# Kernel optimization log

Measured on AMD Instinct MI355X. Metric: run time of the kernel, lower is better.

Reference implementation:

```python
import jax, jax.numpy as jnp
import numpy as np

DIM = 512
NUM_HEADS = 8


def setup_inputs() -> dict:
    key = jax.random.key(0)
    ks = jax.random.split(key, 10)
    B, N, C = 2, 4096, DIM
    s = 0.02
    return {
        "x": jax.random.normal(ks[0], (B, N, C), dtype=jnp.float32),
        "Wq": jax.random.normal(ks[1], (C, C), dtype=jnp.float32) * s,
        "Wk": jax.random.normal(ks[2], (C, C), dtype=jnp.float32) * s,
        "Wv": jax.random.normal(ks[3], (C, C), dtype=jnp.float32) * s,
        "Wattn": jax.random.normal(ks[4], (C, C), dtype=jnp.float32) * s,
        "Wconv": jax.random.normal(ks[5], (C, C), dtype=jnp.float32) * s,
        "dw_kernel": jax.random.normal(ks[6], (C, 1, 3), dtype=jnp.float32) * s,  # depthwise (O, I/groups, K)
        "dw_bias": jax.random.normal(ks[7], (C,), dtype=jnp.float32) * s,
        "Wcout": jax.random.normal(ks[8], (C, C), dtype=jnp.float32) * s,
        "H": 8,
        "W": 512,
    }


def reference(x, Wq, Wk, Wv, Wattn, Wconv, dw_kernel, dw_bias, Wcout, H, W):
    B, N, C = x.shape
    nh = NUM_HEADS
    hd = C // nh
    scale = hd ** (-0.5)

    # QKV projections (torch Linear: x @ W.T), split heads -> [B, nh, N, hd]
    q = (x @ Wq.T).reshape(B, N, nh, hd).transpose(0, 2, 1, 3)
    k = (x @ Wk.T).reshape(B, N, nh, hd).transpose(0, 2, 1, 3)
    v = (x @ Wv.T).reshape(B, N, nh, hd).transpose(0, 2, 1, 3)

    # Materialized N x N attention (faithful to source)
    scores = jnp.einsum("bhqd,bhkd->bhqk", q, k) * scale
    weights = jax.nn.softmax(scores, axis=-1)
    attn = jnp.einsum("bhqk,bhkd->bhqd", weights, v)
    attn = attn.transpose(0, 2, 1, 3).reshape(B, N, C)
    attn_out = attn @ Wattn.T

    # Parallel depthwise-conv branch
    ci = (x @ Wconv.T).transpose(0, 2, 1)  # [B, C, N]
    co = jax.lax.conv_general_dilated(
        ci, dw_kernel,
        window_strides=(1,), padding=((1, 1),),
        feature_group_count=C,
        dimension_numbers=("NCH", "OIH", "NCH"),
    ) + dw_bias[None, :, None]
    conv_out = co.transpose(0, 2, 1) @ Wcout.T  # [B, N, C]

    out = attn_out + conv_out
    # NOTE: source shadows arg H with num_heads before the view
    return out.reshape(B, nh, W, C)
```

## Files before the change

### kernel.cpp

```cpp
#include <hip/hip_runtime.h>

typedef __attribute__((ext_vector_type(8))) short bf16x8;
typedef __attribute__((ext_vector_type(4))) float f32x4;

constexpr int kB = 2, kN = 4096, kC = 512, kNH = 8, kHD = 64;
constexpr int kBN = kB * kN;
constexpr int kWElems = 262144;
constexpr int kWAll = 6 * kWElems;
constexpr int kWExtra = 3584;
constexpr float kQScale = 0.1803368801f;

__device__ __forceinline__ short f2bf(float f) {
  union { float f; unsigned u; } v; v.f = f;
  unsigned r = v.u + 0x7fffu + ((v.u >> 16) & 1u);
  return (short)(r >> 16);
}
__device__ __forceinline__ float bf2f(short s) {
  union { unsigned u; float f; } v; v.u = ((unsigned)(unsigned short)s) << 16;
  return v.f;
}
__device__ __forceinline__ float exp2_(float x) {
#if __has_builtin(__builtin_amdgcn_exp2f)
  return __builtin_amdgcn_exp2f(x);
#else
  return exp2f(x);
#endif
}
__device__ __forceinline__ unsigned pk2bf(float a, float b) {
  union { float f; unsigned u; } ua, ub; ua.f = a; ub.f = b;
#if __has_builtin(__builtin_amdgcn_perm)
  return __builtin_amdgcn_perm(ub.u + 0x8000u, ua.u + 0x8000u, 0x07060302u);
#else
  return ((ua.u + 0x8000u) >> 16) | (((ub.u + 0x8000u) >> 16) << 16);
#endif
}

__device__ __forceinline__ bf16x8 ld8(const short* p) { return *(const bf16x8*)p; }
__device__ __forceinline__ bf16x8 ld8(const float* p) {
  float4 a = *(const float4*)p;
  float4 b = *(const float4*)(p + 4);
  bf16x8 r;
  r[0] = f2bf(a.x); r[1] = f2bf(a.y); r[2] = f2bf(a.z); r[3] = f2bf(a.w);
  r[4] = f2bf(b.x); r[5] = f2bf(b.y); r[6] = f2bf(b.z); r[7] = f2bf(b.w);
  return r;
}
__device__ __forceinline__ void stf(short* p, float v) { *p = f2bf(v); }
__device__ __forceinline__ void stf(float* p, float v) { *p = v; }

__device__ __forceinline__ void gload_lds16(const void* g, void* l) {
  __builtin_amdgcn_global_load_lds(
      (const __attribute__((address_space(1))) void*)g,
      (__attribute__((address_space(3))) void*)l, 16, 0, 0);
}

__global__ void detect_dtype(const unsigned* __restrict__ x, int* __restrict__ flag) {
  const int lane = threadIdx.x & 63;
  unsigned w = x[lane];
  int e = (int)((w >> 7) & 0xffu);
  bool bf = (e >= 100 && e <= 140);
  unsigned long long m = __ballot(bf);
  if (lane == 0) *flag = (__popcll(m) >= 32) ? 1 : 0;
}

constexpr int kW8 = kWAll / 8;
constexpr int kX8 = kBN * kC / 8;
__global__ __launch_bounds__(256) void convert_all(
    const void* Wq, const void* Wk, const void* Wv, const void* Wc,
    const void* Wa, const void* Wco, const void* dwk, const void* dwb,
    const void* x, const int* __restrict__ flag, short* __restrict__ dst,
    short* __restrict__ xb) {
  const int gtid = blockIdx.x * 256 + threadIdx.x;
  const bool bf = (*flag != 0);
  if (gtid < kW8) {
    const int e = gtid * 8;
    const int t = e >> 18, off = e & (kWElems - 1);
    const void* src = (t == 0) ? Wq : (t == 1) ? Wk : (t == 2) ? Wv
                    : (t == 3) ? Wc : (t == 4) ? Wa : Wco;
    bf16x8 v = bf ? ld8((const short*)src + off) : ld8((const float*)src + off);
    *(bf16x8*)(dst + e) = v;
  } else if (gtid < kW8 + kWExtra) {
    const int eoff = gtid - kW8;
    if (eoff < 1536) {
      dst[kWAll + eoff] = bf ? ((const short*)dwk)[eoff]
                             : f2bf(((const float*)dwk)[eoff]);
    } else if (eoff < 2048) {
      const int i = eoff - 1536;
      dst[kWAll + 1536 + i] = bf ? ((const short*)dwb)[i]
                                 : f2bf(((const float*)dwb)[i]);
    } else {
      const int t2 = eoff - 2048;
      const int tap = t2 >> 9, c = t2 & 511;
      dst[kWAll + 2048 + t2] = bf ? ((const short*)dwk)[c * 3 + tap]
                                  : f2bf(((const float*)dwk)[c * 3 + tap]);
    }
  } else if (gtid < kW8 + kWExtra + kX8) {
    const int e = (gtid - kW8 - kWExtra) * 8;
    bf16x8 v = bf ? ld8((const short*)x + e) : ld8((const float*)x + e);
    *(bf16x8*)(xb + e) = v;
  }
}

__global__ __launch_bounds__(256, 3) void proj_gemm(
    const short* __restrict__ xb, const short* __restrict__ wb,
    short* __restrict__ q, short* __restrict__ k, short* __restrict__ vT,
    short* __restrict__ ci) {
  __shared__ __align__(16) short As[128 * 64];
  __shared__ __align__(16) short Bs[128 * 64];
  const int t = threadIdx.x;
  const int wave = t >> 6, lane = t & 63;
  const int row = lane & 15, quad = lane >> 4;
  const int bn = blockIdx.x & 15;
  const int bm = blockIdx.x >> 4;
  const int m0 = bm * 128, n0 = bn * 128;
  const int wm = wave & 1, wn = wave >> 1;
  const int lrow = lane >> 3, lch = lane & 7;

  f32x4 acc[4][4];
#pragma unroll
  for (int mi = 0; mi < 4; ++mi)
#pragma unroll
    for (int ni = 0; ni < 4; ++ni)
#pragma unroll
      for (int r = 0; r < 4; ++r) acc[mi][ni][r] = 0.0f;

  for (int k0 = 0; k0 < kC; k0 += 64) {
#pragma unroll
    for (int p = 0; p < 4; ++p) {
      const int m = wave * 32 + p * 8 + lrow;
      const int kch = lch ^ (m & 7);
      gload_lds16(xb + (size_t)(m0 + m) * kC + k0 + kch * 8,
                  &As[(wave * 32 + p * 8) * 64]);
      gload_lds16(wb + (size_t)(n0 + m) * kC + k0 + kch * 8,
                  &Bs[(wave * 32 + p * 8) * 64]);
    }
    __syncthreads();

#pragma unroll
    for (int kk2 = 0; kk2 < 2; ++kk2) {
      bf16x8 af[4], bfr[4];
#pragma unroll
      for (int mi = 0; mi < 4; ++mi) {
        const int m = wm * 64 + mi * 16 + row;
        const int ch = (kk2 * 4 + quad) ^ (m & 7);
        af[mi] = *(const bf16x8*)(&As[m * 64 + ch * 8]);
      }
#pragma unroll
      for (int ni = 0; ni < 4; ++ni) {
        const int n = wn * 64 + ni * 16 + row;
        const int ch = (kk2 * 4 + quad) ^ (n & 7);
        bfr[ni] = *(const bf16x8*)(&Bs[n * 64 + ch * 8]);
      }
#pragma unroll
      for (int mi = 0; mi < 4; ++mi)
#pragma unroll
        for (int ni = 0; ni < 4; ++ni)
          acc[mi][ni] = __builtin_amdgcn_mfma_f32_16x16x32_bf16(
              af[mi], bfr[ni], acc[mi][ni], 0, 0, 0);
    }
    __syncthreads();
  }

  const int gc0 = n0 + wn * 64;
  const int mat = gc0 >> 9;
  const float scale = (mat == 0) ? kQScale : 1.0f;
#pragma unroll
  for (int mi = 0; mi < 4; ++mi) {
#pragma unroll
    for (int ni = 0; ni < 4; ++ni) {
#pragma unroll
      for (int r = 0; r < 4; ++r) {
        const int gm = m0 + wm * 64 + mi * 16 + quad * 4 + r;
        const int c_ = ((gc0 + ni * 16) & 511) + row;
        const int b_ = gm >> 12;
        const int n_ = gm & (kN - 1);
        const short bv = f2bf(acc[mi][ni][r] * scale);
        if (mat == 3) {
          ci[(b_ * kN + n_) * kC + c_] = bv;
        } else {
          const int h = c_ >> 6, d = c_ & 63;
          const int bh = b_ * kNH + h;
          if (mat == 0)      q[(bh * kN + n_) * kHD + d] = bv;
          else if (mat == 1) k[(bh * kN + n_) * kHD + d] = bv;
          else               vT[(bh * kHD + d) * kN + n_] = bv;
        }
      }
    }
  }
}

__global__ __launch_bounds__(256) void dwconv(
    const short* __restrict__ ci, const short* __restrict__ wb,
    short* __restrict__ cb) {
  const int e0 = (blockIdx.x * 256 + threadIdx.x) * 8;
  const int c0 = e0 & (kC - 1);
  const int bn = e0 >> 9;
  const int n_ = bn & (kN - 1);
  bf16x8 xc = ld8(ci + e0);
  bf16x8 xm, xp;
  if (n_ > 0) xm = ld8(ci + e0 - kC);
  else
#pragma unroll
    for (int i = 0; i < 8; ++i) xm[i] = 0;
  if (n_ < kN - 1) xp = ld8(ci + e0 + kC);
  else
#pragma unroll
    for (int i = 0; i < 8; ++i) xp[i] = 0;
  bf16x8 w0 = ld8(wb + kWAll + 2048 + c0);
  bf16x8 w1 = ld8(wb + kWAll + 2048 + 512 + c0);
  bf16x8 w2 = ld8(wb + kWAll + 2048 + 1024 + c0);
  bf16x8 bi = ld8(wb + kWAll + 1536 + c0);
  bf16x8 o;
#pragma unroll
  for (int i = 0; i < 8; ++i) {
    float a = bf2f(bi[i]) + bf2f(xm[i]) * bf2f(w0[i]) +
              bf2f(xc[i]) * bf2f(w1[i]) + bf2f(xp[i]) * bf2f(w2[i]);
    o[i] = f2bf(a);
  }
  *(bf16x8*)(cb + e0) = o;
}

__global__ __launch_bounds__(256, 3) void attn_flash(
    const short* __restrict__ q, const short* __restrict__ k,
    const short* __restrict__ vT, short* __restrict__ attn) {
  __shared__ __align__(16) short Kb[2][64 * 72];
  __shared__ __align__(16) short VbS[2][64 * 72];
  const int t = threadIdx.x;
  const int wave = t >> 6;
  const int lane = t & 63;
  const int row = lane & 15;
  const int quad = lane >> 4;

  const int slot = blockIdx.x & 7;
  const int inner = blockIdx.x >> 3;
  const int bh = slot * 2 + (inner & 1);
  const int q0 = (inner >> 1) * 128 + wave * 32;

  const short* qbase = q + (bh * kN + q0) * kHD;
  const short* kbase = k + bh * kN * kHD;
  const short* vbase = vT + bh * kHD * kN;

  bf16x8 qb[2][2];
#pragma unroll
  for (int g = 0; g < 2; ++g) {
    qb[g][0] = *(const bf16x8*)(qbase + (g * 16 + row) * kHD + quad * 8);
    qb[g][1] = *(const bf16x8*)(qbase + (g * 16 + row) * kHD + 32 + quad * 8);
  }

  f32x4 o[2][4];
#pragma unroll
  for (int g = 0; g < 2; ++g)
#pragma unroll
    for (int j = 0; j < 4; ++j)
#pragma unroll
      for (int r = 0; r < 4; ++r) o[g][j][r] = 0.0f;
  float l_[2] = {0.0f, 0.0f};

  const int i0 = t, i1 = t + 256;
  const int sr0 = i0 >> 3, sc0 = i0 & 7;
  const int sr1 = i1 >> 3, sc1 = i1 & 7;
  const int vb0 = (sc0 >> 2) * 32 + (sc0 & 1) * 16 + (sc0 & 2) * 2;
  const int vb1 = (sc1 >> 2) * 32 + (sc1 & 1) * 16 + (sc1 & 2) * 2;

  auto stage_v = [&](int buf, bf16x8 v0, bf16x8 v1) {
    *(short4*)(&VbS[buf][sr0 * 72 + vb0]) =
        make_short4(v0[0], v0[1], v0[2], v0[3]);
    *(short4*)(&VbS[buf][sr0 * 72 + vb0 + 8]) =
        make_short4(v0[4], v0[5], v0[6], v0[7]);
    *(short4*)(&VbS[buf][sr1 * 72 + vb1]) =
        make_short4(v1[0], v1[1], v1[2], v1[3]);
    *(short4*)(&VbS[buf][sr1 * 72 + vb1 + 8]) =
        make_short4(v1[4], v1[5], v1[6], v1[7]);
  };

  {
    bf16x8 ka = *(const bf16x8*)(kbase + i0 * 8);
    bf16x8 kb2 = *(const bf16x8*)(kbase + i1 * 8);
    *(bf16x8*)(&Kb[0][sr0 * 72 + sc0 * 8]) = ka;
    *(bf16x8*)(&Kb[0][sr1 * 72 + sc1 * 8]) = kb2;
    bf16x8 v0 = *(const bf16x8*)(vbase + sr0 * kN + sc0 * 8);
    bf16x8 v1 = *(const bf16x8*)(vbase + sr1 * kN + sc1 * 8);
    stage_v(0, v0, v1);
  }
  __syncthreads();

  for (int kt = 0; kt < kN / 64; ++kt) {
    const int cur = kt & 1;
    const bool more = (kt < kN / 64 - 1);
    bf16x8 kn0, kn1, vn0, vn1;
    if (more) {
      kn0 = *(const bf16x8*)(kbase + (kt + 1) * 4096 + i0 * 8);
      kn1 = *(const bf16x8*)(kbase + (kt + 1) * 4096 + i1 * 8);
      vn0 = *(const bf16x8*)(vbase + sr0 * kN + (kt + 1) * 64 + sc0 * 8);
      vn1 = *(const bf16x8*)(vbase + sr1 * kN + (kt + 1) * 64 + sc1 * 8);
    }

    f32x4 s[2][4];
#pragma unroll
    for (int g = 0; g < 2; ++g)
#pragma unroll
      for (int jk = 0; jk < 4; ++jk)
#pragma unroll
        for (int r = 0; r < 4; ++r) s[g][jk][r] = 0.0f;
#pragma unroll
    for (int jk = 0; jk < 4; ++jk) {
      const short* kr = &Kb[cur][(jk * 16 + row) * 72 + quad * 8];
      bf16x8 a0 = *(const bf16x8*)kr;
      bf16x8 a1 = *(const bf16x8*)(kr + 32);
#pragma unroll
      for (int g = 0; g < 2; ++g) {
        s[g][jk] = __builtin_amdgcn_mfma_f32_16x16x32_bf16(a0, qb[g][0], s[g][jk], 0, 0, 0);
        s[g][jk] = __builtin_amdgcn_mfma_f32_16x16x32_bf16(a1, qb[g][1], s[g][jk], 0, 0, 0);
      }
    }

    bf16x8 pb[2][2];
#pragma unroll
    for (int g = 0; g < 2; ++g) {
      float rs = 0.0f;
#pragma unroll
      for (int jk = 0; jk < 4; ++jk)
#pragma unroll
        for (int r = 0; r < 4; ++r) {
          float p = exp2_(s[g][jk][r]);
          s[g][jk][r] = p;
          rs += p;
        }
      l_[g] += rs;
#pragma unroll
      for (int c = 0; c < 2; ++c) {
        union { unsigned u[4]; bf16x8 v; } pu;
        pu.u[0] = pk2bf(s[g][2 * c][0], s[g][2 * c][1]);
        pu.u[1] = pk2bf(s[g][2 * c][2], s[g][2 * c][3]);
        pu.u[2] = pk2bf(s[g][2 * c + 1][0], s[g][2 * c + 1][1]);
        pu.u[3] = pk2bf(s[g][2 * c + 1][2], s[g][2 * c + 1][3]);
        pb[g][c] = pu.v;
      }
    }

#pragma unroll
    for (int jd = 0; jd < 4; ++jd) {
      const short* vb = &VbS[cur][(jd * 16 + row) * 72 + quad * 8];
#pragma unroll
      for (int c = 0; c < 2; ++c) {
        bf16x8 av = *(const bf16x8*)(vb + c * 32);
#pragma unroll
        for (int g = 0; g < 2; ++g)
          o[g][jd] = __builtin_amdgcn_mfma_f32_16x16x32_bf16(
              av, pb[g][c], o[g][jd], 0, 0, 0);
      }
    }

    if (more) {
      *(bf16x8*)(&Kb[1 - cur][sr0 * 72 + sc0 * 8]) = kn0;
      *(bf16x8*)(&Kb[1 - cur][sr1 * 72 + sc1 * 8]) = kn1;
      stage_v(1 - cur, vn0, vn1);
    }
    __syncthreads();
  }

  const int b_ = bh >> 3, h = bh & 7;
#pragma unroll
  for (int g = 0; g < 2; ++g) {
    float lt = l_[g];
    lt += __shfl_xor(lt, 16);
    lt += __shfl_xor(lt, 32);
    const float linv = 1.0f / lt;
    const int n_ = q0 + g * 16 + row;
    short* ob = attn + (b_ * kN + n_) * kC + h * kHD + quad * 4;
#pragma unroll
    for (int jd = 0; jd < 4; ++jd) {
      short4 st = make_short4(f2bf(o[g][jd][0] * linv), f2bf(o[g][jd][1] * linv),
                              f2bf(o[g][jd][2] * linv), f2bf(o[g][jd][3] * linv));
      *(short4*)(ob + jd * 16) = st;
    }
  }
}

template <typename TO>
__device__ __forceinline__ void out_body(
    const short* __restrict__ attn, const short* __restrict__ cb,
    const short* __restrict__ wb, TO* __restrict__ out) {
  __shared__ __align__(16) short As[128 * 64];
  __shared__ __align__(16) short Bs[64 * 64];
  const int t = threadIdx.x;
  const int wave = t >> 6, lane = t & 63;
  const int row = lane & 15, quad = lane >> 4;
  const int bn = blockIdx.x & 7;
  const int bm = blockIdx.x >> 3;
  const int m0 = bm * 128, n0 = bn * 64;
  const int wm = wave & 1, wn = wave >> 1;
  const int lrow = lane >> 3, lch = lane & 7;

  f32x4 acc[4][2];
#pragma unroll
  for (int mi = 0; mi < 4; ++mi)
#pragma unroll
    for (int ni = 0; ni < 2; ++ni)
#pragma unroll
      for (int r = 0; r < 4; ++r) acc[mi][ni][r] = 0.0f;

  const short* Wa = wb + 4 * kWElems;
  const short* Wo = wb + 5 * kWElems;

  for (int k0 = 0; k0 < 1024; k0 += 64) {
    const short* Asrc = (k0 < 512) ? attn : cb;
    const short* Bsrc = (k0 < 512) ? Wa : Wo;
    const int ka = k0 & 511;
#pragma unroll
    for (int p = 0; p < 4; ++p) {
      const int m = wave * 32 + p * 8 + lrow;
      const int kch = lch ^ (m & 7);
      gload_lds16(Asrc + (size_t)(m0 + m) * kC + ka + kch * 8,
                  &As[(wave * 32 + p * 8) * 64]);
    }
#pragma unroll
    for (int p = 0; p < 2; ++p) {
      const int n = wave * 16 + p * 8 + lrow;
      const int kch = lch ^ (n & 7);
      gload_lds16(Bsrc + (size_t)(n0 + n) * kC + ka + kch * 8,
                  &Bs[(wave * 16 + p * 8) * 64]);
    }
    __syncthreads();

#pragma unroll
    for (int kk2 = 0; kk2 < 2; ++kk2) {
      bf16x8 af[4], bfr[2];
#pragma unroll
      for (int mi = 0; mi < 4; ++mi) {
        const int m = wm * 64 + mi * 16 + row;
        const int ch = (kk2 * 4 + quad) ^ (m & 7);
        af[mi] = *(const bf16x8*)(&As[m * 64 + ch * 8]);
      }
#pragma unroll
      for (int ni = 0; ni < 2; ++ni) {
        const int n = wn * 32 + ni * 16 + row;
        const int ch = (kk2 * 4 + quad) ^ (n & 7);
        bfr[ni] = *(const bf16x8*)(&Bs[n * 64 + ch * 8]);
      }
#pragma unroll
      for (int mi = 0; mi < 4; ++mi)
#pragma unroll
        for (int ni = 0; ni < 2; ++ni)
          acc[mi][ni] = __builtin_amdgcn_mfma_f32_16x16x32_bf16(
              af[mi], bfr[ni], acc[mi][ni], 0, 0, 0);
    }
    __syncthreads();
  }

#pragma unroll
  for (int mi = 0; mi < 4; ++mi)
#pragma unroll
    for (int ni = 0; ni < 2; ++ni)
#pragma unroll
      for (int r = 0; r < 4; ++r) {
        const int gm = m0 + wm * 64 + mi * 16 + quad * 4 + r;
        const int gc = n0 + wn * 32 + ni * 16 + row;
        stf(out + (size_t)gm * kC + gc, acc[mi][ni][r]);
      }
}

__global__ __launch_bounds__(256, 4) void out_gemm(
    const short* __restrict__ attn, const short* __restrict__ cb,
    const short* __restrict__ wb, const int* __restrict__ flag, void* out) {
  if (*flag)
    out_body<short>(attn, cb, wb, (short*)out);
  else
    out_body<float>(attn, cb, wb, (float*)out);
}

extern "C" void kernel_launch(void* const* d_in, const int* in_sizes, int n_in,
                              void* d_out, int out_size, void* d_ws, size_t ws_size,
                              hipStream_t stream) {
  const void* x   = d_in[0];
  const void* Wq  = d_in[1];
  const void* Wk  = d_in[2];
  const void* Wv  = d_in[3];
  const void* Wa  = d_in[4];
  const void* Wc  = d_in[5];
  const void* dwk = d_in[6];
  const void* dwb = d_in[7];
  const void* Wco = d_in[8];

  short* ws = (short*)d_ws;
  const size_t E = (size_t)kBN * kC;
  int*   flag = (int*)ws;
  short* wb   = ws + 256;
  short* q    = wb + kWAll + kWExtra;
  short* k    = q + E;
  short* vT   = k + E;
  short* ci   = vT + E;
  short* cb   = ci + E;
  short* attn = ci;
  short* xb   = cb;

  detect_dtype<<<1, 64, 0, stream>>>((const unsigned*)x, flag);
  const int cvt_threads = kW8 + kWExtra + kX8;
  convert_all<<<(cvt_threads + 255) / 256, 256, 0, stream>>>(
      Wq, Wk, Wv, Wc, Wa, Wco, dwk, dwb, x, flag, wb, xb);
  proj_gemm<<<1024, 256, 0, stream>>>(xb, wb, q, k, vT, ci);
  dwconv<<<(kBN * kC) / (256 * 8), 256, 0, stream>>>(ci, wb, cb);
  attn_flash<<<512, 256, 0, stream>>>(q, k, vT, attn);
  out_gemm<<<512, 256, 0, stream>>>(attn, cb, wb, flag, d_out);
}
```

Measured before the change: 245.9 us.

## Split attention keys across two blocks and combine partial outputs

Each wave of the flash-attention kernel now handles 64 query rows instead of 32, so every K/V tile staged in shared memory is reused across more queries. The key range is optionally split in two (split-K) to keep enough blocks in flight, with a new combine kernel summing the two bf16 partial outputs and their row sums. K tiles are loaded straight into LDS with an XOR swizzle instead of padding, and V staging moves to between the QK and PV phases. The costs are higher register pressure (occupancy hint lowered from 3 to 2), an extra kernel launch, and extra global traffic plus bf16 rounding of the unnormalised partial outputs.

```diff
diff --git a/kernel.cpp b/kernel.cpp
--- a/kernel.cpp
+++ b/kernel.cpp
@@ -219,161 +219,181 @@
   *(bf16x8*)(cb + e0) = o;
 }
 
-__global__ __launch_bounds__(256, 3) void attn_flash(
+__global__ __launch_bounds__(256, 2) void attn_flash(
     const short* __restrict__ q, const short* __restrict__ k,
-    const short* __restrict__ vT, short* __restrict__ attn) {
-  __shared__ __align__(16) short Kb[2][64 * 72];
-  __shared__ __align__(16) short VbS[2][64 * 72];
+    const short* __restrict__ vT, short* __restrict__ pO0,
+    short* __restrict__ pO1, float* __restrict__ pl, int S) {
+  __shared__ __align__(16) short Kb[2][64 * 64];
+  __shared__ __align__(16) short Vb[2][64 * 72];
   const int t = threadIdx.x;
-  const int wave = t >> 6;
-  const int lane = t & 63;
-  const int row = lane & 15;
-  const int quad = lane >> 4;
+  const int wave = t >> 6, lane = t & 63;
+  const int row = lane & 15, quad = lane >> 4;
 
   const int slot = blockIdx.x & 7;
   const int inner = blockIdx.x >> 3;
   const int bh = slot * 2 + (inner & 1);
-  const int q0 = (inner >> 1) * 128 + wave * 32;
+  const int ks = (S == 2) ? ((inner >> 1) & 1) : 0;
+  const int qt = (S == 2) ? (inner >> 2) : (inner >> 1);
+  const int q0 = qt * 256 + wave * 64;
+  const int ktN = (S == 2) ? 32 : 64;
+  const int ktBase = ks * ktN;
 
   const short* qbase = q + (bh * kN + q0) * kHD;
   const short* kbase = k + bh * kN * kHD;
   const short* vbase = vT + bh * kHD * kN;
 
-  bf16x8 qb[2][2];
-#pragma unroll
-  for (int g = 0; g < 2; ++g) {
+  bf16x8 qb[4][2];
+#pragma unroll
+  for (int g = 0; g < 4; ++g) {
     qb[g][0] = *(const bf16x8*)(qbase + (g * 16 + row) * kHD + quad * 8);
     qb[g][1] = *(const bf16x8*)(qbase + (g * 16 + row) * kHD + 32 + quad * 8);
   }
 
-  f32x4 o[2][4];
-#pragma unroll
-  for (int g = 0; g < 2; ++g)
+  f32x4 o[4][4];
+#pragma unroll
+  for (int g = 0; g < 4; ++g)
 #pragma unroll
     for (int j = 0; j < 4; ++j)
 #pragma unroll
       for (int r = 0; r < 4; ++r) o[g][j][r] = 0.0f;
-  float l_[2] = {0.0f, 0.0f};
+  float l_[4] = {0.f, 0.f, 0.f, 0.f};
+
+  const int km1 = wave * 16 + (lane >> 3);
+  const int km2 = km1 + 8;
+  const int kc1 = ((lane & 7) ^ (km1 & 7)) * 8;
+  const int kc2 = ((lane & 7) ^ (km2 & 7)) * 8;
 
   const int i0 = t, i1 = t + 256;
   const int sr0 = i0 >> 3, sc0 = i0 & 7;
   const int sr1 = i1 >> 3, sc1 = i1 & 7;
-  const int vb0 = (sc0 >> 2) * 32 + (sc0 & 1) * 16 + (sc0 & 2) * 2;
-  const int vb1 = (sc1 >> 2) * 32 + (sc1 & 1) * 16 + (sc1 & 2) * 2;
-
-  auto stage_v = [&](int buf, bf16x8 v0, bf16x8 v1) {
-    *(short4*)(&VbS[buf][sr0 * 72 + vb0]) =
-        make_short4(v0[0], v0[1], v0[2], v0[3]);
-    *(short4*)(&VbS[buf][sr0 * 72 + vb0 + 8]) =
-        make_short4(v0[4], v0[5], v0[6], v0[7]);
-    *(short4*)(&VbS[buf][sr1 * 72 + vb1]) =
-        make_short4(v1[0], v1[1], v1[2], v1[3]);
-    *(short4*)(&VbS[buf][sr1 * 72 + vb1 + 8]) =
-        make_short4(v1[4], v1[5], v1[6], v1[7]);
-  };
+  const int vd0 = (sc0 >> 2) * 32 + (sc0 & 1) * 16 + (sc0 & 2) * 2;
+  const int vd1 = (sc1 >> 2) * 32 + (sc1 & 1) * 16 + (sc1 & 2) * 2;
 
   {
-    bf16x8 ka = *(const bf16x8*)(kbase + i0 * 8);
-    bf16x8 kb2 = *(const bf16x8*)(kbase + i1 * 8);
-    *(bf16x8*)(&Kb[0][sr0 * 72 + sc0 * 8]) = ka;
-    *(bf16x8*)(&Kb[0][sr1 * 72 + sc1 * 8]) = kb2;
-    bf16x8 v0 = *(const bf16x8*)(vbase + sr0 * kN + sc0 * 8);
-    bf16x8 v1 = *(const bf16x8*)(vbase + sr1 * kN + sc1 * 8);
-    stage_v(0, v0, v1);
+    gload_lds16(kbase + (ktBase * 64 + km1) * 64 + kc1, &Kb[0][(wave * 16) * 64]);
+    gload_lds16(kbase + (ktBase * 64 + km2) * 64 + kc2, &Kb[0][(wave * 16 + 8) * 64]);
+    const short* v0 = vbase + sr0 * kN + ktBase * 64 + sc0 * 8;
+    const short* v1 = vbase + sr1 * kN + ktBase * 64 + sc1 * 8;
+    *(short4*)(&Vb[0][sr0 * 72 + vd0])     = *(const short4*)v0;
+    *(short4*)(&Vb[0][sr0 * 72 + vd0 + 8]) = *(const short4*)(v0 + 4);
+    *(short4*)(&Vb[0][sr1 * 72 + vd1])     = *(const short4*)v1;
+    *(short4*)(&Vb[0][sr1 * 72 + vd1 + 8]) = *(const short4*)(v1 + 4);
   }
   __syncthreads();
 
-  for (int kt = 0; kt < kN / 64; ++kt) {
+  for (int kt = ktBase; kt < ktBase + ktN; ++kt) {
     const int cur = kt & 1;
-    const bool more = (kt < kN / 64 - 1);
-    bf16x8 kn0, kn1, vn0, vn1;
+    const bool more = (kt < ktBase + ktN - 1);
+    short4 vn0a, vn0b, vn1a, vn1b;
     if (more) {
-      kn0 = *(const bf16x8*)(kbase + (kt + 1) * 4096 + i0 * 8);
-      kn1 = *(const bf16x8*)(kbase + (kt + 1) * 4096 + i1 * 8);
-      vn0 = *(const bf16x8*)(vbase + sr0 * kN + (kt + 1) * 64 + sc0 * 8);
-      vn1 = *(const bf16x8*)(vbase + sr1 * kN + (kt + 1) * 64 + sc1 * 8);
-    }
-
-    f32x4 s[2][4];
-#pragma unroll
-    for (int g = 0; g < 2; ++g)
+      gload_lds16(kbase + ((kt + 1) * 64 + km1) * 64 + kc1,
+                  &Kb[1 - cur][(wave * 16) * 64]);
+      gload_lds16(kbase + ((kt + 1) * 64 + km2) * 64 + kc2,
+                  &Kb[1 - cur][(wave * 16 + 8) * 64]);
+      const short* v0 = vbase + sr0 * kN + (kt + 1) * 64 + sc0 * 8;
+      const short* v1 = vbase + sr1 * kN + (kt + 1) * 64 + sc1 * 8;
+      vn0a = *(const short4*)v0; vn0b = *(const short4*)(v0 + 4);
+      vn1a = *(const short4*)v1; vn1b = *(const short4*)(v1 + 4);
+    }
+
+    bf16x8 ka[4][2];
+#pragma unroll
+    for (int jk = 0; jk < 4; ++jk) {
+      const int m = jk * 16 + row;
+      ka[jk][0] = *(const bf16x8*)(&Kb[cur][m * 64 + (quad ^ (m & 7)) * 8]);
+      ka[jk][1] = *(const bf16x8*)(&Kb[cur][m * 64 + ((quad + 4) ^ (m & 7)) * 8]);
+    }
+
+    bf16x8 pb[4][2];
+#pragma unroll
+    for (int g = 0; g < 4; ++g) {
+      f32x4 s[4];
 #pragma unroll
       for (int jk = 0; jk < 4; ++jk)
 #pragma unroll
-        for (int r = 0; r < 4; ++r) s[g][jk][r] = 0.0f;
-#pragma unroll
-    for (int jk = 0; jk < 4; ++jk) {
-      const short* kr = &Kb[cur][(jk * 16 + row) * 72 + quad * 8];
-      bf16x8 a0 = *(const bf16x8*)kr;
-      bf16x8 a1 = *(const bf16x8*)(kr + 32);
-#pragma unroll
-      for (int g = 0; g < 2; ++g) {
-        s[g][jk] = __builtin_amdgcn_mfma_f32_16x16x32_bf16(a0, qb[g][0], s[g][jk], 0, 0, 0);
-        s[g][jk] = __builtin_amdgcn_mfma_f32_16x16x32_bf16(a1, qb[g][1], s[g][jk], 0, 0, 0);
-      }
-    }
-
-    bf16x8 pb[2][2];
-#pragma unroll
-    for (int g = 0; g < 2; ++g) {
+        for (int r = 0; r < 4; ++r) s[jk][r] = 0.0f;
+#pragma unroll
+      for (int jk = 0; jk < 4; ++jk) {
+        s[jk] = __builtin_amdgcn_mfma_f32_16x16x32_bf16(ka[jk][0], qb[g][0], s[jk], 0, 0, 0);
+        s[jk] = __builtin_amdgcn_mfma_f32_16x16x32_bf16(ka[jk][1], qb[g][1], s[jk], 0, 0, 0);
+      }
       float rs = 0.0f;
 #pragma unroll
       for (int jk = 0; jk < 4; ++jk)
 #pragma unroll
         for (int r = 0; r < 4; ++r) {
-          float p = exp2_(s[g][jk][r]);
-          s[g][jk][r] = p;
+          float p = exp2_(s[jk][r]);
+          s[jk][r] = p;
           rs += p;
         }
       l_[g] += rs;
 #pragma unroll
       for (int c = 0; c < 2; ++c) {
         union { unsigned u[4]; bf16x8 v; } pu;
-        pu.u[0] = pk2bf(s[g][2 * c][0], s[g][2 * c][1]);
-        pu.u[1] = pk2bf(s[g][2 * c][2], s[g][2 * c][3]);
-        pu.u[2] = pk2bf(s[g][2 * c + 1][0], s[g][2 * c + 1][1]);
-        pu.u[3] = pk2bf(s[g][2 * c + 1][2], s[g][2 * c + 1][3]);
+        pu.u[0] = pk2bf(s[2 * c][0], s[2 * c][1]);
+        pu.u[1] = pk2bf(s[2 * c][2], s[2 * c][3]);
+        pu.u[2] = pk2bf(s[2 * c + 1][0], s[2 * c + 1][1]);
+        pu.u[3] = pk2bf(s[2 * c + 1][2], s[2 * c + 1][3]);
         pb[g][c] = pu.v;
       }
     }
 
+    if (more) {
+      *(short4*)(&Vb[1 - cur][sr0 * 72 + vd0])     = vn0a;
+      *(short4*)(&Vb[1 - cur][sr0 * 72 + vd0 + 8]) = vn0b;
+      *(short4*)(&Vb[1 - cur][sr1 * 72 + vd1])     = vn1a;
+      *(short4*)(&Vb[1 - cur][sr1 * 72 + vd1 + 8]) = vn1b;
+    }
+
 #pragma unroll
     for (int jd = 0; jd < 4; ++jd) {
-      const short* vb = &VbS[cur][(jd * 16 + row) * 72 + quad * 8];
+      const short* vb = &Vb[cur][(jd * 16 + row) * 72 + quad * 8];
 #pragma unroll
       for (int c = 0; c < 2; ++c) {
         bf16x8 av = *(const bf16x8*)(vb + c * 32);
 #pragma unroll
-        for (int g = 0; g < 2; ++g)
+        for (int g = 0; g < 4; ++g)
           o[g][jd] = __builtin_amdgcn_mfma_f32_16x16x32_bf16(
               av, pb[g][c], o[g][jd], 0, 0, 0);
       }
     }
-
-    if (more) {
-      *(bf16x8*)(&Kb[1 - cur][sr0 * 72 + sc0 * 8]) = kn0;
-      *(bf16x8*)(&Kb[1 - cur][sr1 * 72 + sc1 * 8]) = kn1;
-      stage_v(1 - cur, vn0, vn1);
-    }
     __syncthreads();
   }
 
   const int b_ = bh >> 3, h = bh & 7;
-#pragma unroll
-  for (int g = 0; g < 2; ++g) {
+  short* pO = (ks == 0) ? pO0 : pO1;
+#pragma unroll
+  for (int g = 0; g < 4; ++g) {
     float lt = l_[g];
     lt += __shfl_xor(lt, 16);
     lt += __shfl_xor(lt, 32);
-    const float linv = 1.0f / lt;
     const int n_ = q0 + g * 16 + row;
-    short* ob = attn + (b_ * kN + n_) * kC + h * kHD + quad * 4;
+    short* ob = pO + (b_ * kN + n_) * kC + h * kHD + quad * 4;
+    const float linv = (S == 1) ? (1.0f / lt) : 1.0f;
 #pragma unroll
     for (int jd = 0; jd < 4; ++jd) {
       short4 st = make_short4(f2bf(o[g][jd][0] * linv), f2bf(o[g][jd][1] * linv),
                               f2bf(o[g][jd][2] * linv), f2bf(o[g][jd][3] * linv));
       *(short4*)(ob + jd * 16) = st;
     }
-  }
+    if (S == 2 && quad == 0) pl[ks * 65536 + bh * kN + n_] = lt;
+  }
+}
+
+__global__ __launch_bounds__(256) void attn_combine(
+    short* __restrict__ pO0, const short* __restrict__ pO1,
+    const float* __restrict__ pl) {
+  const int i8 = (blockIdx.x * 256 + threadIdx.x) * 8;
+  const int b_ = i8 >> 21;
+  const int n_ = (i8 >> 9) & (kN - 1);
+  const int c0 = i8 & (kC - 1);
+  const int bh = b_ * kNH + (c0 >> 6);
+  const float rl = 1.0f / (pl[bh * kN + n_] + pl[65536 + bh * kN + n_]);
+  bf16x8 a = ld8(pO0 + i8), b = ld8(pO1 + i8);
+  bf16x8 o;
+#pragma unroll
+  for (int i = 0; i < 8; ++i) o[i] = f2bf((bf2f(a[i]) + bf2f(b[i])) * rl);
+  *(bf16x8*)(pO0 + i8) = o;
 }
 
 template <typename TO>
@@ -492,6 +512,11 @@
   short* cb   = ci + E;
   short* attn = ci;
   short* xb   = cb;
+  float* pl   = (float*)(cb + E);
+  short* pO1  = (short*)(pl) + 262144;
+
+  const size_t needS2 = ((size_t)(pO1 + E) - (size_t)ws);
+  const int S = (ws_size >= needS2) ? 2 : 1;
 
   detect_dtype<<<1, 64, 0, stream>>>((const unsigned*)x, flag);
   const int cvt_threads = kW8 + kWExtra + kX8;
@@ -499,6 +524,8 @@
       Wq, Wk, Wv, Wc, Wa, Wco, dwk, dwb, x, flag, wb, xb);
   proj_gemm<<<1024, 256, 0, stream>>>(xb, wb, q, k, vT, ci);
   dwconv<<<(kBN * kC) / (256 * 8), 256, 0, stream>>>(ci, wb, cb);
-  attn_flash<<<512, 256, 0, stream>>>(q, k, vT, attn);
+  attn_flash<<<S * 256, 256, 0, stream>>>(q, k, vT, attn, pO1, pl, S);
+  if (S == 2)
+    attn_combine<<<(int)(E / 8 / 256), 256, 0, stream>>>(attn, pO1, pl);
   out_gemm<<<512, 256, 0, stream>>>(attn, cb, wb, flag, d_out);
 }
```

After: 264.0 us. 7.4% more time.
